# Optimization experiments

Hardware: AMD Instinct MI355X
Metric: run time of the kernel (lower is better)

The kernel has to match this reference:

```python
import jax, jax.numpy as jnp
import numpy as np

B, A_DIM, B_DIM, HID = 256, 128, 128, 512


def setup_inputs() -> dict:
    key = jax.random.key(0)
    ks = jax.random.split(key, 11)
    s = 0.02
    return {
        "x": jax.random.normal(ks[0], (B, A_DIM), jnp.float32),
        "y": jax.random.normal(ks[1], (B, B_DIM), jnp.float32),
        # First Linear(A+B -> H), weight split into x-part and y-part
        "Wx": jax.random.normal(ks[2], (A_DIM, HID), jnp.float32) * s,
        "Wy": jax.random.normal(ks[3], (B_DIM, HID), jnp.float32) * s,
        "b0": jax.random.normal(ks[4], (HID,), jnp.float32) * s,
        "W1": jax.random.normal(ks[5], (HID, HID), jnp.float32) * s,
        "b1": jax.random.normal(ks[6], (HID,), jnp.float32) * s,
        "W2": jax.random.normal(ks[7], (HID, HID), jnp.float32) * s,
        "b2": jax.random.normal(ks[8], (HID,), jnp.float32) * s,
        "W3": jax.random.normal(ks[9], (HID, 1), jnp.float32) * s,
        "b3": jax.random.normal(ks[10], (1,), jnp.float32) * s,
    }


def reference(x, y, Wx, Wy, b0, W1, b1, W2, b2, W3, b3):
    # Original: pair (i,j) of the *transposed* output scores f(concat(x[i], y[j])).
    # First Linear over the concat decomposes into x- and y-projections summed
    # by broadcast, avoiding the O(B^2 * (A+B)) tiled concat tensor.
    hx = x @ Wx                      # [B, H]
    hy = y @ Wy                      # [B, H]
    h = jax.nn.relu(hx[:, None, :] + hy[None, :, :] + b0)  # [B, B, H]
    h = jax.nn.relu(h @ W1 + b1)     # [B, B, H]
    h = jax.nn.relu(h @ W2 + b2)     # [B, B, H]
    scores = h @ W3 + b3             # [B, B, 1]
    return scores[..., 0]            # [B, B], out[i,j] = f(x[i], y[j])
```

## Files before the change

### kernel.cpp

```cpp
#include <hip/hip_runtime.h>
#include <hip/hip_bf16.h>

#define BSZ 256
#define ADIM 128
#define HID 512
#define MT 64
#define LDH 520

typedef __attribute__((ext_vector_type(8))) short short8;
typedef __attribute__((ext_vector_type(4))) float float4_t;
typedef __attribute__((ext_vector_type(4))) unsigned uint4_t;

__device__ inline short f32_to_bf16_bits(float f) {
    union { float f; unsigned u; } v; v.f = f;
    unsigned u = v.u;
    unsigned r = u + 0x7FFFu + ((u >> 16) & 1u);
    return (short)(r >> 16);
}

__device__ __forceinline__ unsigned cvt_pk_bf16(float lo, float hi) {
    unsigned r;
    asm("v_cvt_pk_bf16_f32 %0, %1, %2" : "=v"(r) : "v"(lo), "v"(hi));
    return r;
}

__global__ __launch_bounds__(512) void prep_kernel(
        const float* __restrict__ x, const float* __restrict__ y,
        const float* __restrict__ Wx, const float* __restrict__ Wy,
        const float* __restrict__ b0, const float* __restrict__ W1,
        const float* __restrict__ W2,
        float* __restrict__ hx, float* __restrict__ hy,
        short* __restrict__ W1p, short* __restrict__ W2p) {
    __shared__ float lds[64 * 65];
    const int tid = threadIdx.x;
    const int bid = blockIdx.x;

    if (bid < 128) {
        const bool isX = bid < 64;
        const int i0 = (isX ? bid : bid - 64) * 4;
        const float* src = isX ? x : y;
        const float* W   = isX ? Wx : Wy;
        float* dst       = isX ? hx : hy;

        const int h = tid;
        const float* r0 = src + i0 * ADIM;
        float s0 = 0.f, s1 = 0.f, s2 = 0.f, s3 = 0.f;
        const float* wcol = W + h;
        #pragma unroll 8
        for (int k = 0; k < ADIM; ++k) {
            float w = wcol[k * HID];
            s0 = fmaf(r0[k], w, s0);
            s1 = fmaf(r0[ADIM + k], w, s1);
            s2 = fmaf(r0[2 * ADIM + k], w, s2);
            s3 = fmaf(r0[3 * ADIM + k], w, s3);
        }
        float bb = isX ? b0[h] : 0.f;
        dst[(i0 + 0) * HID + h] = s0 + bb;
        dst[(i0 + 1) * HID + h] = s1 + bb;
        dst[(i0 + 2) * HID + h] = s2 + bb;
        dst[(i0 + 3) * HID + h] = s3 + bb;
    } else {
        const int tb = bid - 128;
        const bool is1 = tb < 64;
        const int t8 = is1 ? tb : tb - 64;
        const float* Wsrc = is1 ? W1 : W2;
        short* Wdst = is1 ? W1p : W2p;
        const int k0 = (t8 >> 3) * 64;
        const int n0 = (t8 & 7) * 64;

        #pragma unroll
        for (int i = 0; i < 8; ++i) {
            int r = (tid >> 6) + i * 8;
            int c = tid & 63;
            lds[c * 65 + r] = Wsrc[(k0 + r) * HID + n0 + c];
        }
        __syncthreads();

        const int local_s = tid >> 8;
        const int g_local = (tid >> 6) & 3;
        const int lane    = tid & 63;
        const int quad    = lane >> 4;
        const int lq      = lane & 15;
        const int s_glob  = (t8 >> 3) * 2 + local_s;
        const int g_glob  = (t8 & 7) * 4 + g_local;

        const float* srcp = lds + (g_local * 16 + lq) * 65 + local_s * 32 + quad * 8;
        short8 v;
        #pragma unroll
        for (int j = 0; j < 8; ++j) v[j] = f32_to_bf16_bits(srcp[j]);
        *(short8*)(Wdst + ((s_glob * 32 + g_glob) * 64 + lane) * 8) = v;
    }
}

__device__ __forceinline__ void gemm_layer(short* __restrict__ hs,
                                           const short* __restrict__ Wp,
                                           const float* __restrict__ bias,
                                           int wave, int lane) {
    const int quad = lane >> 4;
    const int lq = lane & 15;
    const int n0 = wave * 64;

    float4_t acc[4][4];
    #pragma unroll
    for (int mi = 0; mi < 4; ++mi)
        #pragma unroll
        for (int ni = 0; ni < 4; ++ni)
            acc[mi][ni] = (float4_t){0.f, 0.f, 0.f, 0.f};

    const short* pb = Wp + wave * 2048 + lane * 8;
    const short* abase = hs + lq * LDH + quad * 8;

    short8 bf[2][4];
    #pragma unroll
    for (int ni = 0; ni < 4; ++ni)
        bf[0][ni] = *(const short8*)(pb + ni * 512);

    const short* ps = pb + 16384;

    #pragma unroll
    for (int s = 0; s < 16; ++s) {
        const int cur = s & 1;
        if (s < 15) {
            #pragma unroll
            for (int ni = 0; ni < 4; ++ni)
                bf[cur ^ 1][ni] = *(const short8*)(ps + ni * 512);
            ps += 16384;
        }
        short8 af[4];
        #pragma unroll
        for (int mi = 0; mi < 4; ++mi)
            af[mi] = *(const short8*)(abase + mi * 16 * LDH + s * 32);
        __builtin_amdgcn_s_setprio(1);
        #pragma unroll
        for (int mi = 0; mi < 4; ++mi)
            #pragma unroll
            for (int ni = 0; ni < 4; ++ni)
                acc[mi][ni] = __builtin_amdgcn_mfma_f32_16x16x32_bf16(
                    af[mi], bf[cur][ni], acc[mi][ni], 0, 0, 0);
        __builtin_amdgcn_s_setprio(0);
    }

    float bv[4];
    #pragma unroll
    for (int ni = 0; ni < 4; ++ni) bv[ni] = bias[n0 + ni * 16 + lq];

    __syncthreads();

    #pragma unroll
    for (int ni = 0; ni < 4; ++ni) {
        #pragma unroll
        for (int mi = 0; mi < 4; ++mi) {
            float v0 = fmaxf(acc[mi][ni][0] + bv[ni], 0.f);
            float v1 = fmaxf(acc[mi][ni][1] + bv[ni], 0.f);
            float v2 = fmaxf(acc[mi][ni][2] + bv[ni], 0.f);
            float v3 = fmaxf(acc[mi][ni][3] + bv[ni], 0.f);
            unsigned p01 = cvt_pk_bf16(v0, v1);
            unsigned p23 = cvt_pk_bf16(v2, v3);
            unsigned short* wb = (unsigned short*)hs
                + (mi * 16 + quad * 4) * LDH + n0 + ni * 16 + lq;
            wb[0]        = (unsigned short)p01;
            wb[LDH]      = (unsigned short)(p01 >> 16);
            wb[2 * LDH]  = (unsigned short)p23;
            wb[3 * LDH]  = (unsigned short)(p23 >> 16);
        }
    }
    __syncthreads();
}

__global__ __launch_bounds__(512, 4) void critic_kernel(
    const float* __restrict__ hx, const float* __restrict__ hy,
    const short* __restrict__ W1p, const short* __restrict__ W2p,
    const float* __restrict__ b1, const float* __restrict__ b2,
    const float* __restrict__ W3, const float* __restrict__ b3,
    float* __restrict__ out) {
    __shared__ short hs[MT * LDH];
    __shared__ float psum[64 * 9];

    const int tid = threadIdx.x;
    const int wave = tid >> 6;
    const int lane = tid & 63;
    const int quad = lane >> 4;
    const int lq   = lane & 15;

    const int i0 = (blockIdx.x >> 5) * 8;
    const int j0 = (blockIdx.x & 31) * 8;

    #pragma unroll
    for (int e = tid; e < MT * 64; e += 512) {
        int r = e >> 6;
        int ko = (e & 63) * 8;
        int ti = r >> 3, tj = r & 7;
        const float4_t* px = (const float4_t*)(hx + (i0 + ti) * HID + ko);
        const float4_t* py = (const float4_t*)(hy + (j0 + tj) * HID + ko);
        float4_t a0 = px[0], a1 = px[1];
        float4_t c0 = py[0], c1 = py[1];
        unsigned d0 = cvt_pk_bf16(fmaxf(a0[0] + c0[0], 0.f), fmaxf(a0[1] + c0[1], 0.f));
        unsigned d1 = cvt_pk_bf16(fmaxf(a0[2] + c0[2], 0.f), fmaxf(a0[3] + c0[3], 0.f));
        unsigned d2 = cvt_pk_bf16(fmaxf(a1[0] + c1[0], 0.f), fmaxf(a1[1] + c1[1], 0.f));
        unsigned d3 = cvt_pk_bf16(fmaxf(a1[2] + c1[2], 0.f), fmaxf(a1[3] + c1[3], 0.f));
        *(uint4_t*)(hs + r * LDH + ko) = (uint4_t){d0, d1, d2, d3};
    }
    __syncthreads();

    gemm_layer(hs, W1p, b1, wave, lane);
    gemm_layer(hs, W2p, b2, wave, lane);

    {
        const int n0 = wave * 64;
        union { unsigned u[4]; short8 v; } w3u[2];
        #pragma unroll
        for (int s = 0; s < 2; ++s) {
            float wv[8];
            #pragma unroll
            for (int j = 0; j < 8; ++j)
                wv[j] = (lq == 0) ? W3[n0 + s * 32 + quad * 8 + j] : 0.f;
            #pragma unroll
            for (int j = 0; j < 4; ++j)
                w3u[s].u[j] = cvt_pk_bf16(wv[2 * j], wv[2 * j + 1]);
        }

        float4_t facc[4];
        #pragma unroll
        for (int mi = 0; mi < 4; ++mi) facc[mi] = (float4_t){0.f, 0.f, 0.f, 0.f};

        const short* abase = hs + lq * LDH + n0 + quad * 8;
        #pragma unroll
        for (int s = 0; s < 2; ++s)
            #pragma unroll
            for (int mi = 0; mi < 4; ++mi) {
                short8 af = *(const short8*)(abase + mi * 16 * LDH + s * 32);
                facc[mi] = __builtin_amdgcn_mfma_f32_16x16x32_bf16(
                    af, w3u[s].v, facc[mi], 0, 0, 0);
            }

        if (lq == 0) {
            #pragma unroll
            for (int mi = 0; mi < 4; ++mi)
                #pragma unroll
                for (int r = 0; r < 4; ++r)
                    psum[(mi * 16 + quad * 4 + r) * 9 + wave] = facc[mi][r];
        }
    }
    __syncthreads();
    if (tid < 64) {
        float s = b3[0];
        #pragma unroll
        for (int o = 0; o < 8; ++o) s += psum[tid * 9 + o];
        out[(i0 + (tid >> 3)) * BSZ + (j0 + (tid & 7))] = s;
    }
}

extern "C" void kernel_launch(void* const* d_in, const int* in_sizes, int n_in,
                              void* d_out, int out_size, void* d_ws, size_t ws_size,
                              hipStream_t stream) {
    const float* x  = (const float*)d_in[0];
    const float* y  = (const float*)d_in[1];
    const float* Wx = (const float*)d_in[2];
    const float* Wy = (const float*)d_in[3];
    const float* b0 = (const float*)d_in[4];
    const float* W1 = (const float*)d_in[5];
    const float* b1 = (const float*)d_in[6];
    const float* W2 = (const float*)d_in[7];
    const float* b2 = (const float*)d_in[8];
    const float* W3 = (const float*)d_in[9];
    const float* b3 = (const float*)d_in[10];
    float* out = (float*)d_out;

    char* ws = (char*)d_ws;
    float* hx  = (float*)(ws);
    float* hy  = (float*)(ws + 512 * 1024);
    short* W1p = (short*)(ws + 1024 * 1024);
    short* W2p = (short*)(ws + 1536 * 1024);

    prep_kernel<<<256, 512, 0, stream>>>(x, y, Wx, Wy, b0, W1, W2, hx, hy, W1p, W2p);
    critic_kernel<<<1024, 512, 0, stream>>>(hx, hy, W1p, W2p, b1, b2, W3, b3, out);
}
```

Before: 137.5 us.

## Store LDS activations in MFMA fragment order with permuted lane layout

Replaces the padded row-major LDS activation tile (LDH=520) with a fragment-major layout. Each 16x32 A-fragment occupies a contiguous 512-element block, and lanes are placed through a 6-bit permutation. A-operand reads become contiguous 16-byte loads at (s*4+mi)*512, and the epilogue writes and the initial hx+hy fill are remapped to match. The goal is fewer LDS bank conflicts and simpler addressing, with a slightly smaller LDS footprint, at the cost of more intricate index math that must stay consistent across all three stages.

```diff
diff --git a/kernel.cpp b/kernel.cpp
--- a/kernel.cpp
+++ b/kernel.cpp
@@ -4,8 +4,6 @@
 #define BSZ 256
 #define ADIM 128
 #define HID 512
-#define MT 64
-#define LDH 520
 
 typedef __attribute__((ext_vector_type(8))) short short8;
 typedef __attribute__((ext_vector_type(4))) float float4_t;
@@ -22,6 +20,10 @@
     unsigned r;
     asm("v_cvt_pk_bf16_f32 %0, %1, %2" : "=v"(r) : "v"(lo), "v"(hi));
     return r;
+}
+
+__device__ __forceinline__ int perm6(int l) {
+    return ((l & 12) >> 1) | ((l >> 4) & 1) | ((l & 3) << 3) | (l & 32);
 }
 
 __global__ __launch_bounds__(512) void prep_kernel(
@@ -99,6 +101,7 @@
     const int quad = lane >> 4;
     const int lq = lane & 15;
     const int n0 = wave * 64;
+    const int aoff = perm6(lane) * 8;
 
     float4_t acc[4][4];
     #pragma unroll
@@ -108,7 +111,7 @@
             acc[mi][ni] = (float4_t){0.f, 0.f, 0.f, 0.f};
 
     const short* pb = Wp + wave * 2048 + lane * 8;
-    const short* abase = hs + lq * LDH + quad * 8;
+    const short* abase = hs + aoff;
 
     short8 bf[2][4];
     #pragma unroll
@@ -129,7 +132,7 @@
         short8 af[4];
         #pragma unroll
         for (int mi = 0; mi < 4; ++mi)
-            af[mi] = *(const short8*)(abase + mi * 16 * LDH + s * 32);
+            af[mi] = *(const short8*)(abase + (s * 4 + mi) * 512);
         __builtin_amdgcn_s_setprio(1);
         #pragma unroll
         for (int mi = 0; mi < 4; ++mi)
@@ -146,6 +149,8 @@
 
     __syncthreads();
 
+    unsigned short* wp = (unsigned short*)hs + wave * 4096
+                         + ((quad << 1) + (lq >> 3)) * 8 + (lq & 7);
     #pragma unroll
     for (int ni = 0; ni < 4; ++ni) {
         #pragma unroll
@@ -156,12 +161,11 @@
             float v3 = fmaxf(acc[mi][ni][3] + bv[ni], 0.f);
             unsigned p01 = cvt_pk_bf16(v0, v1);
             unsigned p23 = cvt_pk_bf16(v2, v3);
-            unsigned short* wb = (unsigned short*)hs
-                + (mi * 16 + quad * 4) * LDH + n0 + ni * 16 + lq;
-            wb[0]        = (unsigned short)p01;
-            wb[LDH]      = (unsigned short)(p01 >> 16);
-            wb[2 * LDH]  = (unsigned short)p23;
-            wb[3 * LDH]  = (unsigned short)(p23 >> 16);
+            const int off = ((ni >> 1) * 4 + mi) * 512 + (ni & 1) * 256;
+            wp[off +   0] = (unsigned short)p01;
+            wp[off +  64] = (unsigned short)(p01 >> 16);
+            wp[off + 128] = (unsigned short)p23;
+            wp[off + 192] = (unsigned short)(p23 >> 16);
         }
     }
     __syncthreads();
@@ -173,7 +177,7 @@
     const float* __restrict__ b1, const float* __restrict__ b2,
     const float* __restrict__ W3, const float* __restrict__ b3,
     float* __restrict__ out) {
-    __shared__ short hs[MT * LDH];
+    __shared__ short hs[64 * 512];
     __shared__ float psum[64 * 9];
 
     const int tid = threadIdx.x;
@@ -181,24 +185,27 @@
     const int lane = tid & 63;
     const int quad = lane >> 4;
     const int lq   = lane & 15;
+    const int aoff = perm6(lane) * 8;
 
     const int i0 = (blockIdx.x >> 5) * 8;
     const int j0 = (blockIdx.x & 31) * 8;
 
     #pragma unroll
-    for (int e = tid; e < MT * 64; e += 512) {
-        int r = e >> 6;
-        int ko = (e & 63) * 8;
-        int ti = r >> 3, tj = r & 7;
-        const float4_t* px = (const float4_t*)(hx + (i0 + ti) * HID + ko);
-        const float4_t* py = (const float4_t*)(hy + (j0 + tj) * HID + ko);
+    for (int it = 0; it < 8; ++it) {
+        const int frag = wave + it * 8;
+        const int s  = frag >> 2;
+        const int mi = frag & 3;
+        const int row = mi * 16 + lq;
+        const int k0  = s * 32 + quad * 8;
+        const float4_t* px = (const float4_t*)(hx + (i0 + (row >> 3)) * HID + k0);
+        const float4_t* py = (const float4_t*)(hy + (j0 + (row & 7)) * HID + k0);
         float4_t a0 = px[0], a1 = px[1];
         float4_t c0 = py[0], c1 = py[1];
         unsigned d0 = cvt_pk_bf16(fmaxf(a0[0] + c0[0], 0.f), fmaxf(a0[1] + c0[1], 0.f));
         unsigned d1 = cvt_pk_bf16(fmaxf(a0[2] + c0[2], 0.f), fmaxf(a0[3] + c0[3], 0.f));
         unsigned d2 = cvt_pk_bf16(fmaxf(a1[0] + c1[0], 0.f), fmaxf(a1[1] + c1[1], 0.f));
         unsigned d3 = cvt_pk_bf16(fmaxf(a1[2] + c1[2], 0.f), fmaxf(a1[3] + c1[3], 0.f));
-        *(uint4_t*)(hs + r * LDH + ko) = (uint4_t){d0, d1, d2, d3};
+        *(uint4_t*)(hs + frag * 512 + aoff) = (uint4_t){d0, d1, d2, d3};
     }
     __syncthreads();
 
@@ -206,31 +213,30 @@
     gemm_layer(hs, W2p, b2, wave, lane);
 
     {
-        const int n0 = wave * 64;
         union { unsigned u[4]; short8 v; } w3u[2];
         #pragma unroll
-        for (int s = 0; s < 2; ++s) {
+        for (int s2 = 0; s2 < 2; ++s2) {
             float wv[8];
             #pragma unroll
             for (int j = 0; j < 8; ++j)
-                wv[j] = (lq == 0) ? W3[n0 + s * 32 + quad * 8 + j] : 0.f;
+                wv[j] = (lq == 0) ? W3[wave * 64 + s2 * 32 + quad * 8 + j] : 0.f;
             #pragma unroll
             for (int j = 0; j < 4; ++j)
-                w3u[s].u[j] = cvt_pk_bf16(wv[2 * j], wv[2 * j + 1]);
+                w3u[s2].u[j] = cvt_pk_bf16(wv[2 * j], wv[2 * j + 1]);
         }
 
         float4_t facc[4];
         #pragma unroll
         for (int mi = 0; mi < 4; ++mi) facc[mi] = (float4_t){0.f, 0.f, 0.f, 0.f};
 
-        const short* abase = hs + lq * LDH + n0 + quad * 8;
-        #pragma unroll
-        for (int s = 0; s < 2; ++s)
+        const short* abase = hs + aoff;
+        #pragma unroll
+        for (int s2 = 0; s2 < 2; ++s2)
             #pragma unroll
             for (int mi = 0; mi < 4; ++mi) {
-                short8 af = *(const short8*)(abase + mi * 16 * LDH + s * 32);
+                short8 af = *(const short8*)(abase + ((wave * 2 + s2) * 4 + mi) * 512);
                 facc[mi] = __builtin_amdgcn_mfma_f32_16x16x32_bf16(
-                    af, w3u[s].v, facc[mi], 0, 0, 0);
+                    af, w3u[s2].v, facc[mi], 0, 0, 0);
             }
 
         if (lq == 0) {
```

Result: slower. 147.9 us (+7.5%).

## Switch hidden-layer GEMMs to 32x32x16 bf16 MFMA with matching weight packing

Applied to the files above, without the earlier changes.

Replaces the 4x4 grid of 16x16x32 MFMAs per wave with a 2x2 grid of 32x32x16 MFMAs, and repacks W1/W2 into the operand layout the larger instruction expects. Per-wave A-fragment LDS reads per output drop because each 32-row fragment is reused over more columns, with fewer instructions issued. The cost is more k-steps (32 instead of 16) and a more scattered epilogue write pattern back into LDS.

```diff
diff --git a/kernel.cpp b/kernel.cpp
--- a/kernel.cpp
+++ b/kernel.cpp
@@ -9,6 +9,7 @@
 
 typedef __attribute__((ext_vector_type(8))) short short8;
 typedef __attribute__((ext_vector_type(4))) float float4_t;
+typedef __attribute__((ext_vector_type(16))) float float16_t;
 typedef __attribute__((ext_vector_type(4))) unsigned uint4_t;
 
 __device__ inline short f32_to_bf16_bits(float f) {
@@ -76,19 +77,19 @@
         }
         __syncthreads();
 
-        const int local_s = tid >> 8;
-        const int g_local = (tid >> 6) & 3;
+        const int local_s = tid >> 7;
+        const int g_local = (tid >> 6) & 1;
         const int lane    = tid & 63;
-        const int quad    = lane >> 4;
-        const int lq      = lane & 15;
-        const int s_glob  = (t8 >> 3) * 2 + local_s;
-        const int g_glob  = (t8 & 7) * 4 + g_local;
-
-        const float* srcp = lds + (g_local * 16 + lq) * 65 + local_s * 32 + quad * 8;
+        const int half    = lane >> 5;
+        const int l31     = lane & 31;
+        const int s_glob  = (t8 >> 3) * 4 + local_s;
+        const int g_glob  = (t8 & 7) * 2 + g_local;
+
+        const float* srcp = lds + (g_local * 32 + l31) * 65 + local_s * 16 + half * 8;
         short8 v;
         #pragma unroll
         for (int j = 0; j < 8; ++j) v[j] = f32_to_bf16_bits(srcp[j]);
-        *(short8*)(Wdst + ((s_glob * 32 + g_glob) * 64 + lane) * 8) = v;
+        *(short8*)(Wdst + ((s_glob * 16 + g_glob) * 64 + lane) * 8) = v;
     }
 }
 
@@ -96,72 +97,71 @@
                                            const short* __restrict__ Wp,
                                            const float* __restrict__ bias,
                                            int wave, int lane) {
-    const int quad = lane >> 4;
-    const int lq = lane & 15;
+    const int half = lane >> 5;
+    const int l31 = lane & 31;
     const int n0 = wave * 64;
 
-    float4_t acc[4][4];
-    #pragma unroll
-    for (int mi = 0; mi < 4; ++mi)
-        #pragma unroll
-        for (int ni = 0; ni < 4; ++ni)
-            acc[mi][ni] = (float4_t){0.f, 0.f, 0.f, 0.f};
-
-    const short* pb = Wp + wave * 2048 + lane * 8;
-    const short* abase = hs + lq * LDH + quad * 8;
-
-    short8 bf[2][4];
-    #pragma unroll
-    for (int ni = 0; ni < 4; ++ni)
-        bf[0][ni] = *(const short8*)(pb + ni * 512);
-
-    const short* ps = pb + 16384;
-
-    #pragma unroll
-    for (int s = 0; s < 16; ++s) {
+    float16_t acc[2][2];
+    #pragma unroll
+    for (int mi = 0; mi < 2; ++mi)
+        #pragma unroll
+        for (int ni = 0; ni < 2; ++ni)
+            #pragma unroll
+            for (int r = 0; r < 16; ++r)
+                acc[mi][ni][r] = 0.f;
+
+    const short* pb = Wp + wave * 1024 + lane * 8;
+    const short* abase = hs + l31 * LDH + half * 8;
+
+    short8 bf[2][2];
+    bf[0][0] = *(const short8*)(pb);
+    bf[0][1] = *(const short8*)(pb + 512);
+
+    const short* ps = pb + 8192;
+
+    #pragma unroll
+    for (int s = 0; s < 32; ++s) {
         const int cur = s & 1;
-        if (s < 15) {
-            #pragma unroll
-            for (int ni = 0; ni < 4; ++ni)
-                bf[cur ^ 1][ni] = *(const short8*)(ps + ni * 512);
-            ps += 16384;
-        }
-        short8 af[4];
-        #pragma unroll
-        for (int mi = 0; mi < 4; ++mi)
-            af[mi] = *(const short8*)(abase + mi * 16 * LDH + s * 32);
+        if (s < 31) {
+            bf[cur ^ 1][0] = *(const short8*)(ps);
+            bf[cur ^ 1][1] = *(const short8*)(ps + 512);
+            ps += 8192;
+        }
+        short8 af[2];
+        af[0] = *(const short8*)(abase + s * 16);
+        af[1] = *(const short8*)(abase + 32 * LDH + s * 16);
         __builtin_amdgcn_s_setprio(1);
         #pragma unroll
-        for (int mi = 0; mi < 4; ++mi)
-            #pragma unroll
-            for (int ni = 0; ni < 4; ++ni)
-                acc[mi][ni] = __builtin_amdgcn_mfma_f32_16x16x32_bf16(
+        for (int mi = 0; mi < 2; ++mi)
+            #pragma unroll
+            for (int ni = 0; ni < 2; ++ni)
+                acc[mi][ni] = __builtin_amdgcn_mfma_f32_32x32x16_bf16(
                     af[mi], bf[cur][ni], acc[mi][ni], 0, 0, 0);
         __builtin_amdgcn_s_setprio(0);
     }
 
-    float bv[4];
-    #pragma unroll
-    for (int ni = 0; ni < 4; ++ni) bv[ni] = bias[n0 + ni * 16 + lq];
-
-    __syncthreads();
-
-    #pragma unroll
-    for (int ni = 0; ni < 4; ++ni) {
-        #pragma unroll
-        for (int mi = 0; mi < 4; ++mi) {
-            float v0 = fmaxf(acc[mi][ni][0] + bv[ni], 0.f);
-            float v1 = fmaxf(acc[mi][ni][1] + bv[ni], 0.f);
-            float v2 = fmaxf(acc[mi][ni][2] + bv[ni], 0.f);
-            float v3 = fmaxf(acc[mi][ni][3] + bv[ni], 0.f);
-            unsigned p01 = cvt_pk_bf16(v0, v1);
-            unsigned p23 = cvt_pk_bf16(v2, v3);
+    float bv[2];
+    #pragma unroll
+    for (int ni = 0; ni < 2; ++ni) bv[ni] = bias[n0 + ni * 32 + l31];
+
+    __syncthreads();
+
+    #pragma unroll
+    for (int ni = 0; ni < 2; ++ni) {
+        #pragma unroll
+        for (int mi = 0; mi < 2; ++mi) {
             unsigned short* wb = (unsigned short*)hs
-                + (mi * 16 + quad * 4) * LDH + n0 + ni * 16 + lq;
-            wb[0]        = (unsigned short)p01;
-            wb[LDH]      = (unsigned short)(p01 >> 16);
-            wb[2 * LDH]  = (unsigned short)p23;
-            wb[3 * LDH]  = (unsigned short)(p23 >> 16);
+                + (mi * 32 + 4 * half) * LDH + n0 + ni * 32 + l31;
+            #pragma unroll
+            for (int rp = 0; rp < 8; ++rp) {
+                const int r0 = 2 * rp;
+                const int row_off = ((r0 & 3) + 8 * (r0 >> 2)) * LDH;
+                float v0 = fmaxf(acc[mi][ni][r0] + bv[ni], 0.f);
+                float v1 = fmaxf(acc[mi][ni][r0 + 1] + bv[ni], 0.f);
+                unsigned p = cvt_pk_bf16(v0, v1);
+                wb[row_off]       = (unsigned short)p;
+                wb[row_off + LDH] = (unsigned short)(p >> 16);
+            }
         }
     }
     __syncthreads();
@@ -209,14 +209,14 @@
         const int n0 = wave * 64;
         union { unsigned u[4]; short8 v; } w3u[2];
         #pragma unroll
-        for (int s = 0; s < 2; ++s) {
+        for (int s2 = 0; s2 < 2; ++s2) {
             float wv[8];
             #pragma unroll
             for (int j = 0; j < 8; ++j)
-                wv[j] = (lq == 0) ? W3[n0 + s * 32 + quad * 8 + j] : 0.f;
+                wv[j] = (lq == 0) ? W3[n0 + s2 * 32 + quad * 8 + j] : 0.f;
             #pragma unroll
             for (int j = 0; j < 4; ++j)
-                w3u[s].u[j] = cvt_pk_bf16(wv[2 * j], wv[2 * j + 1]);
+                w3u[s2].u[j] = cvt_pk_bf16(wv[2 * j], wv[2 * j + 1]);
         }
 
         float4_t facc[4];
@@ -225,12 +225,12 @@
 
         const short* abase = hs + lq * LDH + n0 + quad * 8;
         #pragma unroll
-        for (int s = 0; s < 2; ++s)
+        for (int s2 = 0; s2 < 2; ++s2)
             #pragma unroll
             for (int mi = 0; mi < 4; ++mi) {
-                short8 af = *(const short8*)(abase + mi * 16 * LDH + s * 32);
+                short8 af = *(const short8*)(abase + mi * 16 * LDH + s2 * 32);
                 facc[mi] = __builtin_amdgcn_mfma_f32_16x16x32_bf16(
-                    af, w3u[s].v, facc[mi], 0, 0, 0);
+                    af, w3u[s2].v, facc[mi], 0, 0, 0);
             }
 
         if (lq == 0) {
```

Measured after the change: 151.2 us. +10.0%, slower.
